# Optimization experiments

Measured on AMD Instinct MI355X. Metric: run time of the kernel, lower is better.

The kernel has to match this reference:

```python
import jax, jax.numpy as jnp
import numpy as np
from jax import lax

NC = 10        # tess_size
EPS = 1e-07


def cpab_basis(nc):
    # Constraint matrix L @ Avees = 0, Avees = [a0,b0,a1,b1,...] per cell.
    # Continuity at interior knots x_i = i/nc, plus zero-boundary v(0)=v(1)=0.
    L = np.zeros((nc + 1, 2 * nc))
    for i in range(1, nc):
        xi = i / nc
        L[i - 1, 2 * (i - 1):2 * i] = [xi, 1.0]
        L[i - 1, 2 * i:2 * i + 2] = [-xi, -1.0]
    L[nc - 1, 1] = 1.0                      # v(0) = b_0 = 0
    L[nc, 2 * nc - 2:2 * nc] = [1.0, 1.0]   # v(1) = a_{nc-1} + b_{nc-1} = 0
    U, S, Vh = np.linalg.svd(L)
    rank = int((S > 1e-8 * S[0]).sum())
    return np.ascontiguousarray(Vh[rank:].T).astype(np.float32)  # (2*nc, nc-1)


def mlp(x1, W0, b0, W1, b1, W2, b2, W3, b3):
    h = jax.nn.relu(x1 @ W0 + b0)
    h = jax.nn.relu(h @ W1 + b1)
    h = jax.nn.relu(h @ W2 + b2)
    return h @ W3 + b3


def integrate_cpab(x, A, nc):
    # x: [N] in (0,1); A: [N, nc, 2] per-cell (slope a, intercept b).
    # Closed-form integration of dphi/dt = a_c*phi + b_c for t in [0,1],
    # walking across cells. Also accumulates s = integral of a(phi(t)) dt,
    # so dphi/dx = exp(s)  (space gradient of the transform).
    a_all = A[..., 0]
    b_all = A[..., 1]
    fnc = jnp.asarray(nc, x.dtype)
    c0 = jnp.clip(jnp.floor(x * nc).astype(jnp.int32), 0, nc - 1)

    def step(carry, _):
        phi, c, t, s, done = carry
        a = jnp.take_along_axis(a_all, c[:, None], 1)[:, 0]
        b = jnp.take_along_axis(b_all, c[:, None], 1)[:, 0]
        v = a * phi + b
        big = jnp.abs(a) > 1e-10
        a_safe = jnp.where(big, a, 1.0)
        # closed-form solution with remaining time t
        psi = jnp.where(big, (phi + b / a_safe) * jnp.exp(a * t) - b / a_safe,
                        phi + b * t)
        lo = c.astype(x.dtype) / fnc
        hi = (c + 1).astype(x.dtype) / fnc
        inside = (psi >= lo) & (psi <= hi)
        xc = jnp.where(v >= 0, hi, lo)          # boundary hit in flow direction
        vb = a * xc + b
        v_safe = jnp.where(v == 0, 1.0, v)
        ratio = jnp.maximum(vb / v_safe, 1e-30)
        t_hit = jnp.where(big, jnp.log(ratio) / a_safe, (xc - phi) / v_safe)
        act = ~done
        cross = act & ~inside
        s = s + jnp.where(act, a * jnp.where(inside, t, t_hit), 0.0)
        phi = jnp.where(cross, xc, jnp.where(act & inside, psi, phi))
        t = jnp.where(cross, t - t_hit, t)
        c = jnp.clip(jnp.where(cross, c + jnp.where(v >= 0, 1, -1), c), 0, nc - 1)
        done = done | inside
        return (phi, c, t, s, done), None

    init = (x, c0, jnp.ones_like(x), jnp.zeros_like(x),
            jnp.zeros(x.shape, bool))
    (phi, _, _, s, _), _ = lax.scan(step, init, None, length=nc + 1)
    return phi, jnp.exp(s)


def _forward(x, B, W0, b0, W1, b1, W2, b2, W3, b3):
    mask = jnp.array([1, 0])  # left=True
    x = jnp.clip(x, EPS, 1.0 - EPS)
    xm = x[:, mask]
    x1, x2 = xm[:, :1], xm[:, 1:]          # [N,1] each
    theta = mlp(x1, W0, b0, W1, b1, W2, b2, W3, b3)   # [N, nc-1]
    A = (theta @ B.T).reshape(-1, NC, 2)    # per-cell (a, b)
    z2, dz2 = integrate_cpab(x2[:, 0], A, NC)
    z = jnp.column_stack([x1[:, 0], z2])[:, mask]
    log_dz_dx = jnp.column_stack([jnp.zeros_like(x1[:, 0]),
                                  jnp.log(dz2)])[:, mask]
    return z, log_dz_dx


def setup_inputs() -> dict:
    key = jax.random.key(0)
    ks = jax.random.split(key, 9)
    N, H, D = 4_194_304, 10, NC - 1
    x = jax.random.uniform(ks[0], (N, 2), jnp.float32)
    sc = 0.5
    return {
        'x': x,
        'B': jnp.asarray(cpab_basis(NC)),
        'W0': jax.random.normal(ks[1], (1, H), jnp.float32) * sc,
        'b0': jax.random.normal(ks[2], (H,), jnp.float32) * 0.1,
        'W1': jax.random.normal(ks[3], (H, H), jnp.float32) * sc,
        'b1': jax.random.normal(ks[4], (H,), jnp.float32) * 0.1,
        'W2': jax.random.normal(ks[5], (H, H), jnp.float32) * sc,
        'b2': jax.random.normal(ks[6], (H,), jnp.float32) * 0.1,
        'W3': jax.random.normal(ks[7], (H, D), jnp.float32) * sc,
        'b3': jax.random.normal(ks[8], (D,), jnp.float32) * 0.1,
    }


def reference(x, B, W0, b0, W1, b1, W2, b2, W3, b3):
    return _forward(x, B, W0, b0, W1, b1, W2, b2, W3, b3)
```

## Files before the change

kernel.cpp:

```cpp
#include <hip/hip_runtime.h>
#include <math.h>

#define NCELL 10
#define TPTS  512
#define BLK   1024
#define PCOLS 13

__device__ __forceinline__ float satf(float v) {
    return fminf(fmaxf(v, -3.389e38f), 3.389e38f);
}

__global__ __launch_bounds__(256) void table_kernel(
    const float* __restrict__ B,
    const float* __restrict__ W0, const float* __restrict__ b0,
    const float* __restrict__ W1, const float* __restrict__ b1,
    const float* __restrict__ W2, const float* __restrict__ b2,
    const float* __restrict__ W3, const float* __restrict__ b3,
    float* __restrict__ tab, float lo, float hi, float dx)
{
    const int i = blockIdx.x * 256 + threadIdx.x;
    if (i >= TPTS) return;
    float x1 = fmaf((float)i, dx, lo);
    if (i == TPTS - 1) x1 = hi;

    float h0[10], h1[10], h2[10];
    #pragma unroll
    for (int j = 0; j < 10; ++j)
        h0[j] = fmaxf(fmaf(x1, W0[j], b0[j]), 0.0f);
    #pragma unroll
    for (int j = 0; j < 10; ++j) {
        float acc = b1[j];
        #pragma unroll
        for (int k = 0; k < 10; ++k) acc = fmaf(h0[k], W1[k * 10 + j], acc);
        h1[j] = fmaxf(acc, 0.0f);
    }
    #pragma unroll
    for (int j = 0; j < 10; ++j) {
        float acc = b2[j];
        #pragma unroll
        for (int k = 0; k < 10; ++k) acc = fmaf(h1[k], W2[k * 10 + j], acc);
        h2[j] = fmaxf(acc, 0.0f);
    }
    float theta[9];
    #pragma unroll
    for (int j = 0; j < 9; ++j) {
        float acc = b3[j];
        #pragma unroll
        for (int k = 0; k < 10; ++k) acc = fmaf(h2[k], W3[k * 9 + j], acc);
        theta[j] = acc;
    }
    #pragma unroll
    for (int j = 1; j <= 9; ++j) {
        float aj = 0.f, bj = 0.f;
        #pragma unroll
        for (int q = 0; q < 9; ++q) {
            aj = fmaf(theta[q], B[(2 * j) * 9 + q], aj);
            bj = fmaf(theta[q], B[(2 * j + 1) * 9 + q], bj);
        }
        tab[(j - 1) * TPTS + i] = fmaf(aj, (float)j / 10.0f, bj);
    }
}

__global__ __launch_bounds__(BLK) void cpab_kernel(
    const float* __restrict__ x,
    const float* __restrict__ tab,
    float* __restrict__ out, int N,
    float lo, float inv_dx)
{
    __shared__ float sT[PCOLS * TPTS];

    const int tid = threadIdx.x;

    {
        const float4* g4 = reinterpret_cast<const float4*>(tab);
        float4* s4 = reinterpret_cast<float4*>(sT);
        const int real_lo = 2 * TPTS / 4;
        const int real_hi = 11 * TPTS / 4;
        #pragma unroll
        for (int k = tid; k < PCOLS * TPTS / 4; k += BLK) {
            const bool real = (k >= real_lo) && (k < real_hi);
            s4[k] = real ? g4[k - real_lo] : make_float4(0.f, 0.f, 0.f, 0.f);
        }
    }
    __syncthreads();

    const int i = blockIdx.x * BLK + tid;
    if (i >= N) return;

    const float2 xv = reinterpret_cast<const float2*>(x)[i];
    const float hi_clip = 1.0f - 1e-7f;
    const float x2 = fminf(fmaxf(xv.x, 1e-7f), hi_clip);
    const float x1 = fminf(fmaxf(xv.y, 1e-7f), hi_clip);

    const float tt  = (x1 - lo) * inv_dx;
    const int  cell = min((int)tt, TPTS - 2);
    const float f   = tt - (float)cell;

    const float* base = sT + cell;
    auto node = [&](int j) -> float {
        const float* pp = base + (j + 1) * TPTS;
        return fmaf(f, pp[1] - pp[0], pp[0]);
    };

    const float p10  = x2 * 10.0f;
    const int   cc0  = (int)p10;
    const float frac = p10 - (float)cc0;
    const float nc = node(cc0);
    const float nn = node(cc0 + 1);
    const float a0s = (nn - nc) * 10.0f;
    const float u0 = fmaf(nn - nc, frac, nc);
    const bool  right = (u0 >= 0.0f);
    const float d10   = right ? 10.0f : -10.0f;
    const int   dint  = right ? 1 : -1;

    float p  = x2;
    float u  = u0;
    float ru = __builtin_amdgcn_rcpf(u0);
    int   cn = cc0 + (right ? 1 : 0);
    float w  = right ? nn : nc;
    float wnext = node(cn + dint);
    float t  = 1.0f;
    float a  = 0.0f, ra = 1.0f;
    bool  big = false;

    #pragma unroll 1
    for (int it = 0; ; ++it) {
        a   = (w - u) * d10;
        big = fabsf(a) > 1e-10f;
        ra  = __builtin_amdgcn_rcpf(big ? a : 1.0f);
        const float q  = w * ru;
        const float lg = __logf(q);
        const float xc = (float)cn * 0.1f;
        const float t_hit = big ? (lg * ra) : ((xc - p) * ru);
        if (!(t_hit < t) || it >= 11) break;
        t  -= t_hit;
        p   = xc;
        u   = w;
        ru  = __builtin_amdgcn_rcpf(w);
        cn += dint;
        w   = wnext;
        wnext = node(cn + dint);
    }

    const float e   = __expf(a * t);
    float phi = big ? fmaf(u * ra, e - 1.0f, p) : fmaf(u, t, p);
    const float ru0 = __builtin_amdgcn_rcpf(u0);
    float ldz = __logf(fabsf(u * e * ru0));
    if (u0 == 0.0f) { phi = x2; ldz = a0s; }

    reinterpret_cast<float2*>(out)[i] = make_float2(satf(phi), x1);
    reinterpret_cast<float2*>(out + (size_t)2 * N)[i] = make_float2(satf(ldz), 0.0f);
}

extern "C" void kernel_launch(void* const* d_in, const int* in_sizes, int n_in,
                              void* d_out, int out_size, void* d_ws, size_t ws_size,
                              hipStream_t stream) {
    (void)n_in; (void)out_size; (void)ws_size;
    const float* x  = (const float*)d_in[0];
    const float* B  = (const float*)d_in[1];
    const float* W0 = (const float*)d_in[2];
    const float* b0 = (const float*)d_in[3];
    const float* W1 = (const float*)d_in[4];
    const float* b1 = (const float*)d_in[5];
    const float* W2 = (const float*)d_in[6];
    const float* b2 = (const float*)d_in[7];
    const float* W3 = (const float*)d_in[8];
    const float* b3 = (const float*)d_in[9];
    float* ws  = (float*)d_ws;
    float* out = (float*)d_out;

    const int N = in_sizes[0] / 2;
    const float lo = 1e-7f, hi = 1.0f - 1e-7f;
    const float dx = (hi - lo) / (float)(TPTS - 1);
    const float inv_dx = (float)(TPTS - 1) / (hi - lo);

    table_kernel<<<(TPTS + 255) / 256, 256, 0, stream>>>(
        B, W0, b0, W1, b1, W2, b2, W3, b3, ws, lo, hi, dx);
    cpab_kernel<<<(N + BLK - 1) / BLK, BLK, 0, stream>>>(
        x, ws, out, N, lo, inv_dx);
}
```

Measured before the change: 122.7 us.

## Compact straggler lanes into per-wave pool to cut divergent cell-walk iterations

```diff
diff --git a/kernel.cpp b/kernel.cpp
--- a/kernel.cpp
+++ b/kernel.cpp
@@ -3,11 +3,57 @@
 
 #define NCELL 10
 #define TPTS  512
-#define BLK   1024
+#define BLK   512
+#define GRID  768
 #define PCOLS 13
+#define ACT_MIN 32
 
 __device__ __forceinline__ float satf(float v) {
     return fminf(fmaxf(v, -3.389e38f), 3.389e38f);
+}
+
+__device__ __forceinline__ int nth_set_lane(unsigned long long m, int r) {
+    int pos = 0;
+    #pragma unroll
+    for (int b = 32; b >= 1; b >>= 1) {
+        const unsigned long long mask = ((1ull << b) - 1ull) << pos;
+        const int c = __popcll(m & mask);
+        if (r >= c) { r -= c; pos += b; }
+    }
+    return pos;
+}
+
+__device__ __forceinline__ float nodef(const float* base, float f, int j) {
+    const float* pp = base + (j + 1) * TPTS;
+    return fmaf(f, pp[1] - pp[0], pp[0]);
+}
+
+__device__ __forceinline__ void wstep(
+    const float* base, float f, float d10, int dint, int it,
+    float& p, float& u, float& ru, int& cn, float& w,
+    float& t, float& a, float& ra, bool& big, bool& act)
+{
+    const float a_n  = (w - u) * d10;
+    const bool  b_n  = fabsf(a_n) > 1e-10f;
+    const float ra_n = __builtin_amdgcn_rcpf(b_n ? a_n : 1.0f);
+    const float q    = w * ru;
+    const float lg   = __logf(q);
+    const float xc   = (float)cn * 0.1f;
+    const float th   = b_n ? (lg * ra_n) : ((xc - p) * ru);
+    a   = act ? a_n  : a;
+    big = act ? b_n  : big;
+    ra  = act ? ra_n : ra;
+    const bool step = act && (th < t) && (it < 11);
+    t  = step ? t - th : t;
+    p  = step ? xc : p;
+    u  = step ? w  : u;
+    ru = step ? __builtin_amdgcn_rcpf(w) : ru;
+    const int cnn = cn + dint;
+    const int cf  = min(max(cnn, -1), 11);
+    const float wn = nodef(base, f, cf);
+    cn  = step ? cnn : cn;
+    w   = step ? wn  : w;
+    act = step;
 }
 
 __global__ __launch_bounds__(256) void table_kernel(
@@ -61,7 +107,7 @@
     }
 }
 
-__global__ __launch_bounds__(BLK) void cpab_kernel(
+__global__ __launch_bounds__(BLK, 6) void cpab_kernel(
     const float* __restrict__ x,
     const float* __restrict__ tab,
     float* __restrict__ out, int N,
@@ -84,72 +130,128 @@
     }
     __syncthreads();
 
-    const int i = blockIdx.x * BLK + tid;
-    if (i >= N) return;
-
-    const float2 xv = reinterpret_cast<const float2*>(x)[i];
+    const int lane = tid & 63;
     const float hi_clip = 1.0f - 1e-7f;
-    const float x2 = fminf(fmaxf(xv.x, 1e-7f), hi_clip);
-    const float x1 = fminf(fmaxf(xv.y, 1e-7f), hi_clip);
-
-    const float tt  = (x1 - lo) * inv_dx;
-    const int  cell = min((int)tt, TPTS - 2);
-    const float f   = tt - (float)cell;
-
-    const float* base = sT + cell;
-    auto node = [&](int j) -> float {
-        const float* pp = base + (j + 1) * TPTS;
-        return fmaf(f, pp[1] - pp[0], pp[0]);
+
+    int poolcnt = 0;
+    float Pp = 0.f, Pu = 1.f, Pru = 1.f, Pw = 0.f, Pt = 0.f;
+    float Pf = 0.f, Pu0 = 1.f, Px1 = 0.f;
+    int Pcell = 0, Pcn = 0, Pidx = 0;
+
+    auto flush = [&]() {
+        const bool pv = lane < poolcnt;
+        bool act = pv;
+        float p = Pp, u = Pu, ru = Pru, w = Pw, t = Pt, f = Pf, u0 = Pu0;
+        int   cn = Pcn;
+        const float* base = sT + Pcell;
+        const float d10 = (u0 >= 0.f) ? 10.f : -10.f;
+        const int  dint = (u0 >= 0.f) ? 1 : -1;
+        float a = 0.f, ra = 1.f;
+        bool big = false;
+        #pragma unroll 1
+        for (int it = 0; it < 12; ++it) {
+            if (!__any(act)) break;
+            wstep(base, f, d10, dint, it, p, u, ru, cn, w, t, a, ra, big, act);
+        }
+        if (pv) {
+            const float e = __expf(a * t);
+            float phi = big ? fmaf(u * ra, e - 1.0f, p) : fmaf(u, t, p);
+            const float ru0 = __builtin_amdgcn_rcpf(u0);
+            float ldz = __logf(fabsf(u * e * ru0));
+            reinterpret_cast<float2*>(out)[Pidx] = make_float2(satf(phi), Px1);
+            reinterpret_cast<float2*>(out + (size_t)2 * N)[Pidx] =
+                make_float2(satf(ldz), 0.0f);
+        }
     };
 
-    const float p10  = x2 * 10.0f;
-    const int   cc0  = (int)p10;
-    const float frac = p10 - (float)cc0;
-    const float nc = node(cc0);
-    const float nn = node(cc0 + 1);
-    const float a0s = (nn - nc) * 10.0f;
-    const float u0 = fmaf(nn - nc, frac, nc);
-    const bool  right = (u0 >= 0.0f);
-    const float d10   = right ? 10.0f : -10.0f;
-    const int   dint  = right ? 1 : -1;
-
-    float p  = x2;
-    float u  = u0;
-    float ru = __builtin_amdgcn_rcpf(u0);
-    int   cn = cc0 + (right ? 1 : 0);
-    float w  = right ? nn : nc;
-    float wnext = node(cn + dint);
-    float t  = 1.0f;
-    float a  = 0.0f, ra = 1.0f;
-    bool  big = false;
+    const int stride = GRID * BLK;
+    const int nchunks = (N + stride - 1) / stride;
 
     #pragma unroll 1
-    for (int it = 0; ; ++it) {
-        a   = (w - u) * d10;
-        big = fabsf(a) > 1e-10f;
-        ra  = __builtin_amdgcn_rcpf(big ? a : 1.0f);
-        const float q  = w * ru;
-        const float lg = __logf(q);
-        const float xc = (float)cn * 0.1f;
-        const float t_hit = big ? (lg * ra) : ((xc - p) * ru);
-        if (!(t_hit < t) || it >= 11) break;
-        t  -= t_hit;
-        p   = xc;
-        u   = w;
-        ru  = __builtin_amdgcn_rcpf(w);
-        cn += dint;
-        w   = wnext;
-        wnext = node(cn + dint);
-    }
-
-    const float e   = __expf(a * t);
-    float phi = big ? fmaf(u * ra, e - 1.0f, p) : fmaf(u, t, p);
-    const float ru0 = __builtin_amdgcn_rcpf(u0);
-    float ldz = __logf(fabsf(u * e * ru0));
-    if (u0 == 0.0f) { phi = x2; ldz = a0s; }
-
-    reinterpret_cast<float2*>(out)[i] = make_float2(satf(phi), x1);
-    reinterpret_cast<float2*>(out + (size_t)2 * N)[i] = make_float2(satf(ldz), 0.0f);
+    for (int c = 0; c < nchunks; ++c) {
+        const int i = c * stride + blockIdx.x * BLK + tid;
+        const bool valid = i < N;
+        const float2 xv = valid ? reinterpret_cast<const float2*>(x)[i]
+                                : make_float2(0.5f, 0.5f);
+        const float x2 = fminf(fmaxf(xv.x, 1e-7f), hi_clip);
+        const float x1 = fminf(fmaxf(xv.y, 1e-7f), hi_clip);
+
+        const float ttv  = (x1 - lo) * inv_dx;
+        const int  cellv = min((int)ttv, TPTS - 2);
+        const float f    = ttv - (float)cellv;
+        const float* base = sT + cellv;
+
+        const float p10  = x2 * 10.0f;
+        const int   cc0  = (int)p10;
+        const float frac = p10 - (float)cc0;
+        const float nc = nodef(base, f, cc0);
+        const float nn = nodef(base, f, cc0 + 1);
+        const float a0s = (nn - nc) * 10.0f;
+        const float u0 = fmaf(nn - nc, frac, nc);
+        const bool  right = (u0 >= 0.0f);
+        const float d10   = right ? 10.0f : -10.0f;
+        const int   dint  = right ? 1 : -1;
+
+        float p = x2, u = u0;
+        float ru = __builtin_amdgcn_rcpf(u0);
+        int   cn = cc0 + (right ? 1 : 0);
+        float w  = right ? nn : nc;
+        float t = 1.0f, a = 0.0f, ra = 1.0f;
+        bool big = false, act = valid;
+
+        #pragma unroll 1
+        for (int it = 0; it < 12; ++it) {
+            wstep(base, f, d10, dint, it, p, u, ru, cn, w, t, a, ra, big, act);
+            const int nact = __popcll(__ballot(act));
+            if (nact < ACT_MIN) break;
+        }
+
+        const unsigned long long mdef = __ballot(act);
+        const int ns = __popcll(mdef);
+        if (ns > 0) {
+            if (poolcnt + ns > 64) { flush(); poolcnt = 0; }
+            const int r   = lane - poolcnt;
+            const int rc  = min(max(r, 0), 63);
+            const int src = nth_set_lane(mdef, rc);
+            const bool take = (r >= 0) && (r < ns);
+            const float np  = __shfl(p,  src);
+            const float nu  = __shfl(u,  src);
+            const float nru = __shfl(ru, src);
+            const float nw  = __shfl(w,  src);
+            const float nt  = __shfl(t,  src);
+            const float nf  = __shfl(f,  src);
+            const float nu0 = __shfl(u0, src);
+            const float nx1 = __shfl(x1, src);
+            const int ncell = __shfl(cellv, src);
+            const int ncn   = __shfl(cn, src);
+            const int nidx  = __shfl(i,  src);
+            Pp   = take ? np   : Pp;
+            Pu   = take ? nu   : Pu;
+            Pru  = take ? nru  : Pru;
+            Pw   = take ? nw   : Pw;
+            Pt   = take ? nt   : Pt;
+            Pf   = take ? nf   : Pf;
+            Pu0  = take ? nu0  : Pu0;
+            Px1  = take ? nx1  : Px1;
+            Pcell = take ? ncell : Pcell;
+            Pcn   = take ? ncn   : Pcn;
+            Pidx  = take ? nidx  : Pidx;
+            poolcnt += ns;
+        }
+
+        if (valid && !act) {
+            const float e = __expf(a * t);
+            float phi = big ? fmaf(u * ra, e - 1.0f, p) : fmaf(u, t, p);
+            const float ru0 = __builtin_amdgcn_rcpf(u0);
+            float ldz = __logf(fabsf(u * e * ru0));
+            if (u0 == 0.0f) { phi = x2; ldz = a0s; }
+            reinterpret_cast<float2*>(out)[i] = make_float2(satf(phi), x1);
+            reinterpret_cast<float2*>(out + (size_t)2 * N)[i] =
+                make_float2(satf(ldz), 0.0f);
+        }
+    }
+
+    if (poolcnt > 0) flush();
 }
 
 extern "C" void kernel_launch(void* const* d_in, const int* in_sizes, int n_in,
@@ -176,6 +278,6 @@
 
     table_kernel<<<(TPTS + 255) / 256, 256, 0, stream>>>(
         B, W0, b0, W1, b1, W2, b2, W3, b3, ws, lo, hi, dx);
-    cpab_kernel<<<(N + BLK - 1) / BLK, BLK, 0, stream>>>(
+    cpab_kernel<<<GRID, BLK, 0, stream>>>(
         x, ws, out, N, lo, inv_dx);
 }
```

New measurement: 124.5 us. No clear change (+1.4%).
